# Optimization experiments

Measured on AMD Instinct MI355X. Metric: run time of the kernel, lower is better.

Reference implementation:

```python
import jax, jax.numpy as jnp
import numpy as np

B, S, H = 1, 2048, 1024
NH, NKV, HD = 16, 4, 64  # n_attn_heads, n_kv_heads, head_dim


def setup_inputs() -> dict:
    key = jax.random.key(0)
    k1, k2, k3, k4 = jax.random.split(key, 4)
    x = jax.random.normal(k1, (B, S, H), dtype=jnp.float32)
    Wq = jax.random.normal(k2, (H, H), dtype=jnp.float32) * 0.02
    Wk = jax.random.normal(k3, (NKV * HD, H), dtype=jnp.float32) * 0.02
    Wv = jax.random.normal(k4, (NKV * HD, H), dtype=jnp.float32) * 0.02
    return {"x": x, "Wq": Wq, "Wk": Wk, "Wv": Wv}


def reference(x, Wq, Wk, Wv):
    b, s, h = x.shape
    rep = NH // NKV
    # projections (torch Linear: x @ W.T)
    q = (x @ Wq.T).reshape(b, s, NH, HD).transpose(0, 2, 1, 3)      # [b, NH, s, d]
    k = (x @ Wk.T).reshape(b, s, NKV, HD).transpose(0, 2, 1, 3)     # [b, NKV, s, d]
    v = (x @ Wv.T).reshape(b, s, NKV, HD).transpose(0, 2, 1, 3)
    # repeat_kv: expand each kv head rep times
    k = jnp.repeat(k, rep, axis=1)                                   # [b, NH, s, d]
    v = jnp.repeat(v, rep, axis=1)
    # NOTE: source scales by 1/sqrt(hidden_size), not 1/sqrt(head_dim)
    scale = 1.0 / np.sqrt(H).astype(np.float32)
    scores = jnp.einsum('bhqd,bhkd->bhqk', q, k) * scale             # [b, NH, s, s]
    causal = jnp.tril(jnp.ones((s, s), dtype=bool))
    scores = jnp.where(causal[None, None], scores, -jnp.inf)
    probs = jax.nn.softmax(scores, axis=-1)
    y = jnp.einsum('bhqk,bhkd->bhqd', probs, v)                      # [b, NH, s, d]
    return y.transpose(0, 2, 1, 3).reshape(b, s, NH * HD)
```

## Files before the change

kernel.cpp:

```cpp
#include <hip/hip_runtime.h>

#define S_LEN 2048
#define HID   1024
#define NHEAD 16
#define NKVH  4
#define HDIM  64
#define QKSTR 1280

typedef __bf16 bf16x8 __attribute__((ext_vector_type(8)));
typedef __bf16 bf16x4 __attribute__((ext_vector_type(4)));
typedef float  f32x4  __attribute__((ext_vector_type(4)));
typedef short  s16x4  __attribute__((ext_vector_type(4)));

#define QSCALE 0.04508422f

__device__ __forceinline__ unsigned short f2bf(float f) {
    unsigned u = __builtin_bit_cast(unsigned, f);
    u = u + 0x7FFFu + ((u >> 16) & 1u);
    return (unsigned short)(u >> 16);
}

__device__ __forceinline__ bf16x8 cvt8(float4 a, float4 b) {
    bf16x8 r;
    r[0] = (__bf16)a.x; r[1] = (__bf16)a.y; r[2] = (__bf16)a.z; r[3] = (__bf16)a.w;
    r[4] = (__bf16)b.x; r[5] = (__bf16)b.y; r[6] = (__bf16)b.z; r[7] = (__bf16)b.w;
    return r;
}

__device__ __forceinline__ f32x4 mfma_16x16x16_bf16(s16x4 a, s16x4 b, f32x4 c) {
#if __has_builtin(__builtin_amdgcn_mfma_f32_16x16x16bf16_1k)
    return __builtin_amdgcn_mfma_f32_16x16x16bf16_1k(a, b, c, 0, 0, 0);
#else
    f32x4 d = c;
    asm volatile("s_nop 1\n\tv_mfma_f32_16x16x16_bf16 %0, %1, %2, %0\n\ts_nop 3"
                 : "+v"(d) : "v"(a), "v"(b));
    return d;
#endif
}

__global__ __launch_bounds__(256, 2) void proj_gemm(
    const float* __restrict__ x,  const float* __restrict__ wq,
    const float* __restrict__ wk, const float* __restrict__ wv,
    unsigned short* __restrict__ qkv,
    unsigned short* __restrict__ vT)
{
    __shared__ unsigned short At[2][64 * 64];
    __shared__ unsigned short Bt[2][96 * 64];
    const int tid = threadIdx.x;
    const int w = tid >> 6, l = tid & 63;
    const int quad = l >> 4, lane16 = l & 15;
    const int m0 = blockIdx.y * 64, n0 = blockIdx.x * 96;
    const int wm = (w & 1) * 32, wn = (w >> 1) * 48;

    const int srow = l >> 3;
    const int scol = ((l & 7) ^ srow) * 8;
    const int dcol = (l & 7) * 8;

    f32x4 acc[2][3] = {};
    float4 arA[2][2], arB[3][2];

    #define PLOAD(KT)                                                                   \
        do {                                                                            \
            _Pragma("unroll")                                                           \
            for (int c = 0; c < 2; ++c) {                                               \
                const float* ga = x + (long)(m0 + w * 16 + c * 8 + srow) * HID          \
                                    + (KT) + scol;                                      \
                arA[c][0] = ((const float4*)ga)[0];                                     \
                arA[c][1] = ((const float4*)ga)[1];                                     \
            }                                                                           \
            _Pragma("unroll")                                                           \
            for (int c = 0; c < 3; ++c) {                                               \
                const int row = n0 + w * 24 + c * 8 + srow;                             \
                const float* gb = (row < 1024) ? wq + (long)row * HID                   \
                                : (row < 1280) ? wk + (long)(row - 1024) * HID          \
                                               : wv + (long)(row - 1280) * HID;         \
                gb += (KT) + scol;                                                      \
                arB[c][0] = ((const float4*)gb)[0];                                     \
                arB[c][1] = ((const float4*)gb)[1];                                     \
            }                                                                           \
        } while (0)

    #define PWRITE(BUF)                                                                 \
        do {                                                                            \
            _Pragma("unroll")                                                           \
            for (int c = 0; c < 2; ++c)                                                 \
                *(bf16x8*)&At[BUF][(w * 16 + c * 8 + srow) * 64 + dcol] =               \
                    cvt8(arA[c][0], arA[c][1]);                                         \
            _Pragma("unroll")                                                           \
            for (int c = 0; c < 3; ++c)                                                 \
                *(bf16x8*)&Bt[BUF][(w * 24 + c * 8 + srow) * 64 + dcol] =               \
                    cvt8(arB[c][0], arB[c][1]);                                         \
        } while (0)

    PLOAD(0);

    for (int i = 0; i < 16; ++i) {
        const int cur = i & 1;
        PWRITE(cur);
        __syncthreads();
        if (i + 1 < 16) PLOAD((i + 1) * 64);

        #pragma unroll
        for (int ks = 0; ks < 2; ++ks) {
            const int swz = ((ks * 4 + quad) ^ (lane16 & 7)) * 8;
            bf16x8 a[2], b[3];
            #pragma unroll
            for (int mi = 0; mi < 2; ++mi)
                a[mi] = *(const bf16x8*)&At[cur][(wm + mi * 16 + lane16) * 64 + swz];
            #pragma unroll
            for (int ni = 0; ni < 3; ++ni)
                b[ni] = *(const bf16x8*)&Bt[cur][(wn + ni * 16 + lane16) * 64 + swz];
            #pragma unroll
            for (int mi = 0; mi < 2; ++mi)
                #pragma unroll
                for (int ni = 0; ni < 3; ++ni)
                    acc[mi][ni] = __builtin_amdgcn_mfma_f32_16x16x32_bf16(a[mi], b[ni], acc[mi][ni], 0, 0, 0);
        }
    }
    #undef PLOAD
    #undef PWRITE

    #pragma unroll
    for (int mi = 0; mi < 2; ++mi) {
        const int row = m0 + wm + mi * 16 + quad * 4;
        #pragma unroll
        for (int ni = 0; ni < 3; ++ni) {
            const int col = n0 + wn + ni * 16 + lane16;
            #pragma unroll
            for (int r = 0; r < 4; ++r) {
                const float v = acc[mi][ni][r];
                if (col < 1024)
                    qkv[(long)(row + r) * QKSTR + col] = f2bf(v * QSCALE);
                else if (col < 1280)
                    qkv[(long)(row + r) * QKSTR + col] = f2bf(v);
                else
                    vT[(long)(col - 1280) * S_LEN + (row + r)] = f2bf(v);
            }
        }
    }
}

#define KSTR 72
__global__ __launch_bounds__(256, 2) void attn(
    const unsigned short* __restrict__ qkv,
    const unsigned short* __restrict__ vT,
    float* __restrict__ out)
{
    __shared__ unsigned short Kt[4][64 * KSTR];
    __shared__ unsigned short Vt[4][64 * KSTR];

    const int tid = threadIdx.x;
    const int w = tid >> 6, l = tid & 63;
    const int quad = l >> 4, lane16 = l & 15;
    const int bx = blockIdx.x, by = blockIdx.y;
    const int qt = (by & 8) ? (31 - bx) : bx;
    const int h  = by;
    const int kh = h >> 2;
    const int qcol = h * 64;
    const int kcol = 1024 + kh * 64;

    const long qrow = (long)(qt * 64 + w * 16 + lane16);
    bf16x8 qa0 = *(const bf16x8*)&qkv[qrow * QKSTR + qcol + quad * 8];
    bf16x8 qa1 = *(const bf16x8*)&qkv[qrow * QKSTR + qcol + 32 + quad * 8];

    f32x4 oT[4] = {};
    float rsum[4] = {0.f, 0.f, 0.f, 0.f};

    const int sr = tid >> 2, ss = tid & 3;
    const long vrow = (long)(kh * 64 + sr) * S_LEN;

    const int nt = qt + 1;

    bf16x8 kr00, kr01, vr00, vr01;
    bf16x8 kr10, kr11, vr10, vr11;

    #define LOADSLOT0(T)                                                        \
        do {                                                                    \
            const long gk = (long)((T) * 64 + sr) * QKSTR + kcol + ss * 16;     \
            kr00 = *(const bf16x8*)&qkv[gk];                                    \
            kr01 = *(const bf16x8*)&qkv[gk + 8];                                \
            const long gv = vrow + (T) * 64 + ss * 16;                          \
            vr00 = *(const bf16x8*)&vT[gv];                                     \
            vr01 = *(const bf16x8*)&vT[gv + 8];                                 \
        } while (0)
    #define LOADSLOT1(T)                                                        \
        do {                                                                    \
            const long gk = (long)((T) * 64 + sr) * QKSTR + kcol + ss * 16;     \
            kr10 = *(const bf16x8*)&qkv[gk];                                    \
            kr11 = *(const bf16x8*)&qkv[gk + 8];                                \
            const long gv = vrow + (T) * 64 + ss * 16;                          \
            vr10 = *(const bf16x8*)&vT[gv];                                     \
            vr11 = *(const bf16x8*)&vT[gv + 8];                                 \
        } while (0)

    LOADSLOT0(0);
    if (nt > 1) LOADSLOT1(1);

    auto compute = [&](int buf, int tile) {
        f32x4 sacc[4] = {};
        __builtin_amdgcn_s_setprio(1);
        #pragma unroll
        for (int t = 0; t < 4; ++t) {
            bf16x8 kb0 = *(const bf16x8*)&Kt[buf][(t * 16 + lane16) * KSTR + quad * 8];
            bf16x8 kb1 = *(const bf16x8*)&Kt[buf][(t * 16 + lane16) * KSTR + 32 + quad * 8];
            sacc[t] = __builtin_amdgcn_mfma_f32_16x16x32_bf16(kb0, qa0, sacc[t], 0, 0, 0);
            sacc[t] = __builtin_amdgcn_mfma_f32_16x16x32_bf16(kb1, qa1, sacc[t], 0, 0, 0);
        }
        __builtin_amdgcn_s_setprio(0);

        if (tile == qt) {
            #pragma unroll
            for (int t = 0; t < 4; ++t) {
                const int kvw = t * 16 + quad * 4;
                #pragma unroll
                for (int r = 0; r < 4; ++r)
                    if (kvw + r > w * 16 + lane16) sacc[t][r] = -3.0e38f;
            }
        }

        s16x4 pfrag[4];
        #pragma unroll
        for (int t = 0; t < 4; ++t) {
            const float p0 = __builtin_amdgcn_exp2f(sacc[t][0]);
            const float p1 = __builtin_amdgcn_exp2f(sacc[t][1]);
            const float p2 = __builtin_amdgcn_exp2f(sacc[t][2]);
            const float p3 = __builtin_amdgcn_exp2f(sacc[t][3]);
            rsum[t] += (p0 + p1) + (p2 + p3);
            bf16x4 pk;
            pk[0] = (__bf16)p0; pk[1] = (__bf16)p1;
            pk[2] = (__bf16)p2; pk[3] = (__bf16)p3;
            pfrag[t] = __builtin_bit_cast(s16x4, pk);
        }

        __builtin_amdgcn_s_setprio(1);
        #pragma unroll
        for (int dt = 0; dt < 4; ++dt)
            #pragma unroll
            for (int t = 0; t < 4; ++t) {
                bf16x4 va = *(const bf16x4*)&Vt[buf][(dt * 16 + lane16) * KSTR + t * 16 + quad * 4];
                oT[dt] = mfma_16x16x16_bf16(__builtin_bit_cast(s16x4, va), pfrag[t], oT[dt]);
            }
        __builtin_amdgcn_s_setprio(0);
    };

    for (int j = 0; 2 * j < nt; ++j) {
        const int t0 = 2 * j, t1 = 2 * j + 1;
        const bool has1 = (t1 < nt);
        const int p = (j & 1) << 1;

        *(bf16x8*)&Kt[p][sr * KSTR + ss * 16]     = kr00;
        *(bf16x8*)&Kt[p][sr * KSTR + ss * 16 + 8] = kr01;
        *(bf16x8*)&Vt[p][sr * KSTR + ss * 16]     = vr00;
        *(bf16x8*)&Vt[p][sr * KSTR + ss * 16 + 8] = vr01;
        if (has1) {
            *(bf16x8*)&Kt[p + 1][sr * KSTR + ss * 16]     = kr10;
            *(bf16x8*)&Kt[p + 1][sr * KSTR + ss * 16 + 8] = kr11;
            *(bf16x8*)&Vt[p + 1][sr * KSTR + ss * 16]     = vr10;
            *(bf16x8*)&Vt[p + 1][sr * KSTR + ss * 16 + 8] = vr11;
        }
        __syncthreads();

        if (t0 + 2 < nt) LOADSLOT0(t0 + 2);
        if (t1 + 2 < nt) LOADSLOT1(t1 + 2);

        compute(p, t0);
        if (has1) compute(p + 1, t1);
    }
    #undef LOADSLOT0
    #undef LOADSLOT1

    float total = (rsum[0] + rsum[1]) + (rsum[2] + rsum[3]);
    total += __shfl_xor(total, 16);
    total += __shfl_xor(total, 32);
    const float invt = 1.0f / total;

    const long orow_q = (long)(qt * 64 + w * 16 + lane16);
    #pragma unroll
    for (int dt = 0; dt < 4; ++dt) {
        const int col = h * 64 + dt * 16 + quad * 4;
        #pragma unroll
        for (int r = 0; r < 4; ++r)
            out[orow_q * (NHEAD * HDIM) + col + r] = oT[dt][r] * invt;
    }
}

extern "C" void kernel_launch(void* const* d_in, const int* in_sizes, int n_in,
                              void* d_out, int out_size, void* d_ws, size_t ws_size,
                              hipStream_t stream) {
    const float* x  = (const float*)d_in[0];
    const float* wq = (const float*)d_in[1];
    const float* wk = (const float*)d_in[2];
    const float* wv = (const float*)d_in[3];
    float* out = (float*)d_out;

    unsigned short* qkv = (unsigned short*)d_ws;
    unsigned short* vT  = qkv + (size_t)S_LEN * QKSTR;

    proj_gemm<<<dim3(16, 32), dim3(256), 0, stream>>>(x, wq, wk, wv, qkv, vT);
    attn<<<dim3(32, 16), dim3(256), 0, stream>>>(qkv, vT, out);
}
```

Before: 117.2 us.

## Split attention KV range across two blocks and combine partials in a separate kernel

Each query tile's causal KV range is split in half across a new grid z dimension. Each half writes unnormalized partial outputs and row sums to workspace, and a new combine kernel adds them and normalizes. No running max is needed because the scores are pre-scaled and bounded. The goal is to double the number of blocks and shorten the longest blocks, which should improve load balance and occupancy; the LDS buffering drops to two stages and launch bounds are raised to 4 to match. In exchange there is an extra kernel launch and extra global traffic for the fp32 partials.

Result: faster. 114.4 us (-2.4%).

```diff
diff --git a/kernel.cpp b/kernel.cpp
--- a/kernel.cpp
+++ b/kernel.cpp
@@ -141,24 +141,30 @@
 }
 
 #define KSTR 72
-__global__ __launch_bounds__(256, 2) void attn(
+__global__ __launch_bounds__(256, 4) void attn(
     const unsigned short* __restrict__ qkv,
     const unsigned short* __restrict__ vT,
-    float* __restrict__ out)
+    float* __restrict__ opart,
+    float* __restrict__ rpart)
 {
-    __shared__ unsigned short Kt[4][64 * KSTR];
-    __shared__ unsigned short Vt[4][64 * KSTR];
+    __shared__ unsigned short Kt[2][64 * KSTR];
+    __shared__ unsigned short Vt[2][64 * KSTR];
 
     const int tid = threadIdx.x;
     const int w = tid >> 6, l = tid & 63;
     const int quad = l >> 4, lane16 = l & 15;
-    const int bx = blockIdx.x, by = blockIdx.y;
+    const int bx = blockIdx.x, by = blockIdx.y, bz = blockIdx.z;
     const int qt = (by & 8) ? (31 - bx) : bx;
     const int h  = by;
     const int kh = h >> 2;
     const int qcol = h * 64;
     const int kcol = 1024 + kh * 64;
 
+    const int nt  = qt + 1;
+    const int h1  = (nt + 1) >> 1;
+    const int tlo = bz ? h1 : 0;
+    const int thi = bz ? nt : h1;
+
     const long qrow = (long)(qt * 64 + w * 16 + lane16);
     bf16x8 qa0 = *(const bf16x8*)&qkv[qrow * QKSTR + qcol + quad * 8];
     bf16x8 qa1 = *(const bf16x8*)&qkv[qrow * QKSTR + qcol + 32 + quad * 8];
@@ -169,46 +175,46 @@
     const int sr = tid >> 2, ss = tid & 3;
     const long vrow = (long)(kh * 64 + sr) * S_LEN;
 
-    const int nt = qt + 1;
-
-    bf16x8 kr00, kr01, vr00, vr01;
-    bf16x8 kr10, kr11, vr10, vr11;
-
-    #define LOADSLOT0(T)                                                        \
-        do {                                                                    \
-            const long gk = (long)((T) * 64 + sr) * QKSTR + kcol + ss * 16;     \
-            kr00 = *(const bf16x8*)&qkv[gk];                                    \
-            kr01 = *(const bf16x8*)&qkv[gk + 8];                                \
-            const long gv = vrow + (T) * 64 + ss * 16;                          \
-            vr00 = *(const bf16x8*)&vT[gv];                                     \
-            vr01 = *(const bf16x8*)&vT[gv + 8];                                 \
-        } while (0)
-    #define LOADSLOT1(T)                                                        \
-        do {                                                                    \
-            const long gk = (long)((T) * 64 + sr) * QKSTR + kcol + ss * 16;     \
-            kr10 = *(const bf16x8*)&qkv[gk];                                    \
-            kr11 = *(const bf16x8*)&qkv[gk + 8];                                \
-            const long gv = vrow + (T) * 64 + ss * 16;                          \
-            vr10 = *(const bf16x8*)&vT[gv];                                     \
-            vr11 = *(const bf16x8*)&vT[gv + 8];                                 \
-        } while (0)
-
-    LOADSLOT0(0);
-    if (nt > 1) LOADSLOT1(1);
-
-    auto compute = [&](int buf, int tile) {
+    bf16x8 kr0, kr1, vr0, vr1;
+    if (tlo < thi) {
+        const long gk = (long)(tlo * 64 + sr) * QKSTR + kcol + ss * 16;
+        kr0 = *(const bf16x8*)&qkv[gk];
+        kr1 = *(const bf16x8*)&qkv[gk + 8];
+        const long gv = vrow + tlo * 64 + ss * 16;
+        vr0 = *(const bf16x8*)&vT[gv];
+        vr1 = *(const bf16x8*)&vT[gv + 8];
+    }
+
+    for (int kt = tlo; kt < thi; ++kt) {
+        const int cur = kt & 1;
+        *(bf16x8*)&Kt[cur][sr * KSTR + ss * 16]     = kr0;
+        *(bf16x8*)&Kt[cur][sr * KSTR + ss * 16 + 8] = kr1;
+        *(bf16x8*)&Vt[cur][sr * KSTR + ss * 16]     = vr0;
+        *(bf16x8*)&Vt[cur][sr * KSTR + ss * 16 + 8] = vr1;
+
+        __syncthreads();
+
+        if (kt + 1 < thi) {
+            const long gk = (long)((kt + 1) * 64 + sr) * QKSTR + kcol + ss * 16;
+            kr0 = *(const bf16x8*)&qkv[gk];
+            kr1 = *(const bf16x8*)&qkv[gk + 8];
+            const long gv = vrow + (kt + 1) * 64 + ss * 16;
+            vr0 = *(const bf16x8*)&vT[gv];
+            vr1 = *(const bf16x8*)&vT[gv + 8];
+        }
+
         f32x4 sacc[4] = {};
         __builtin_amdgcn_s_setprio(1);
         #pragma unroll
         for (int t = 0; t < 4; ++t) {
-            bf16x8 kb0 = *(const bf16x8*)&Kt[buf][(t * 16 + lane16) * KSTR + quad * 8];
-            bf16x8 kb1 = *(const bf16x8*)&Kt[buf][(t * 16 + lane16) * KSTR + 32 + quad * 8];
+            bf16x8 kb0 = *(const bf16x8*)&Kt[cur][(t * 16 + lane16) * KSTR + quad * 8];
+            bf16x8 kb1 = *(const bf16x8*)&Kt[cur][(t * 16 + lane16) * KSTR + 32 + quad * 8];
             sacc[t] = __builtin_amdgcn_mfma_f32_16x16x32_bf16(kb0, qa0, sacc[t], 0, 0, 0);
             sacc[t] = __builtin_amdgcn_mfma_f32_16x16x32_bf16(kb1, qa1, sacc[t], 0, 0, 0);
         }
         __builtin_amdgcn_s_setprio(0);
 
-        if (tile == qt) {
+        if (kt == qt) {
             #pragma unroll
             for (int t = 0; t < 4; ++t) {
                 const int kvw = t * 16 + quad * 4;
@@ -237,51 +243,46 @@
         for (int dt = 0; dt < 4; ++dt)
             #pragma unroll
             for (int t = 0; t < 4; ++t) {
-                bf16x4 va = *(const bf16x4*)&Vt[buf][(dt * 16 + lane16) * KSTR + t * 16 + quad * 4];
+                bf16x4 va = *(const bf16x4*)&Vt[cur][(dt * 16 + lane16) * KSTR + t * 16 + quad * 4];
                 oT[dt] = mfma_16x16x16_bf16(__builtin_bit_cast(s16x4, va), pfrag[t], oT[dt]);
             }
         __builtin_amdgcn_s_setprio(0);
-    };
-
-    for (int j = 0; 2 * j < nt; ++j) {
-        const int t0 = 2 * j, t1 = 2 * j + 1;
-        const bool has1 = (t1 < nt);
-        const int p = (j & 1) << 1;
-
-        *(bf16x8*)&Kt[p][sr * KSTR + ss * 16]     = kr00;
-        *(bf16x8*)&Kt[p][sr * KSTR + ss * 16 + 8] = kr01;
-        *(bf16x8*)&Vt[p][sr * KSTR + ss * 16]     = vr00;
-        *(bf16x8*)&Vt[p][sr * KSTR + ss * 16 + 8] = vr01;
-        if (has1) {
-            *(bf16x8*)&Kt[p + 1][sr * KSTR + ss * 16]     = kr10;
-            *(bf16x8*)&Kt[p + 1][sr * KSTR + ss * 16 + 8] = kr11;
-            *(bf16x8*)&Vt[p + 1][sr * KSTR + ss * 16]     = vr10;
-            *(bf16x8*)&Vt[p + 1][sr * KSTR + ss * 16 + 8] = vr11;
-        }
-        __syncthreads();
-
-        if (t0 + 2 < nt) LOADSLOT0(t0 + 2);
-        if (t1 + 2 < nt) LOADSLOT1(t1 + 2);
-
-        compute(p, t0);
-        if (has1) compute(p + 1, t1);
-    }
-    #undef LOADSLOT0
-    #undef LOADSLOT1
+    }
 
     float total = (rsum[0] + rsum[1]) + (rsum[2] + rsum[3]);
     total += __shfl_xor(total, 16);
     total += __shfl_xor(total, 32);
-    const float invt = 1.0f / total;
-
-    const long orow_q = (long)(qt * 64 + w * 16 + lane16);
+
+    float* op = opart + (long)bz * S_LEN * (NHEAD * HDIM);
     #pragma unroll
     for (int dt = 0; dt < 4; ++dt) {
         const int col = h * 64 + dt * 16 + quad * 4;
-        #pragma unroll
-        for (int r = 0; r < 4; ++r)
-            out[orow_q * (NHEAD * HDIM) + col + r] = oT[dt][r] * invt;
-    }
+        float4 v; v.x = oT[dt][0]; v.y = oT[dt][1]; v.z = oT[dt][2]; v.w = oT[dt][3];
+        *(float4*)&op[qrow * (NHEAD * HDIM) + col] = v;
+    }
+    if (l < 16)
+        rpart[(long)bz * NHEAD * S_LEN + (long)h * S_LEN + qrow] = total;
+}
+
+__global__ __launch_bounds__(256) void combine(
+    const float* __restrict__ opart, const float* __restrict__ rpart,
+    float* __restrict__ out)
+{
+    const long idx = (long)blockIdx.x * 256 + threadIdx.x;
+    const long row = idx >> 8;
+    const int  c4  = (int)(idx & 255);
+    const int  col = c4 * 4;
+    const int  h   = col >> 6;
+
+    const float4 a = *(const float4*)&opart[row * 1024 + col];
+    const float4 b = *(const float4*)&opart[(long)S_LEN * 1024 + row * 1024 + col];
+    const float r  = rpart[(long)h * S_LEN + row] +
+                     rpart[(long)NHEAD * S_LEN + (long)h * S_LEN + row];
+    const float inv = 1.0f / r;
+    float4 o;
+    o.x = (a.x + b.x) * inv; o.y = (a.y + b.y) * inv;
+    o.z = (a.z + b.z) * inv; o.w = (a.w + b.w) * inv;
+    *(float4*)&out[row * 1024 + col] = o;
 }
 
 extern "C" void kernel_launch(void* const* d_in, const int* in_sizes, int n_in,
@@ -295,7 +296,10 @@
 
     unsigned short* qkv = (unsigned short*)d_ws;
     unsigned short* vT  = qkv + (size_t)S_LEN * QKSTR;
+    float* opart = (float*)(vT + (size_t)256 * S_LEN);
+    float* rpart = opart + (size_t)2 * S_LEN * (NHEAD * HDIM);
 
     proj_gemm<<<dim3(16, 32), dim3(256), 0, stream>>>(x, wq, wk, wv, qkv, vT);
-    attn<<<dim3(32, 16), dim3(256), 0, stream>>>(qkv, vT, out);
-}
+    attn<<<dim3(32, 16, 2), dim3(256), 0, stream>>>(qkv, vT, opart, rpart);
+    combine<<<dim3(2048), dim3(256), 0, stream>>>(opart, rpart, out);
+}
```
